# Optimization experiments

Hardware: AMD Instinct MI355X
Metric: run time of the kernel (lower is better)

The kernel has to match this reference:

```python
import jax, jax.numpy as jnp
import numpy as np

N_NODES = 50000
N_EDGES = 819200  # divisible by num_rels=8 -> equal relation segments (implicit rel_ptr)
NUM_RELS = 8
N_HEADS = 4
IN_FEAT = 256
OUT_FEAT = 128
HEAD_DIM = OUT_FEAT // N_HEADS
LEAKY_SLOPE = 0.2


def setup_inputs() -> dict:
    key = jax.random.key(0)
    ks = jax.random.split(key, 7)
    inputs = jax.random.normal(ks[0], (N_NODES, IN_FEAT), dtype=jnp.float32)
    conv_weights = jax.random.normal(ks[1], (NUM_RELS, N_HEADS, IN_FEAT, HEAD_DIM), dtype=jnp.float32) * (1.0 / np.sqrt(IN_FEAT))
    attn_l = jax.random.normal(ks[2], (NUM_RELS, N_HEADS, HEAD_DIM), dtype=jnp.float32) * 0.1
    attn_r = jax.random.normal(ks[3], (NUM_RELS, N_HEADS, HEAD_DIM), dtype=jnp.float32) * 0.1
    h_bias = jax.random.normal(ks[4], (OUT_FEAT,), dtype=jnp.float32) * 0.01
    row_idx = jax.random.randint(ks[5], (N_EDGES,), 0, N_NODES, dtype=jnp.int32)
    col_idx = jax.random.randint(ks[6], (N_EDGES,), 0, N_NODES, dtype=jnp.int32)
    return {
        'inputs': inputs,
        'conv_weights': conv_weights,
        'attn_l': attn_l,
        'attn_r': attn_r,
        'h_bias': h_bias,
        'row_idx': row_idx,
        'col_idx': col_idx,
    }


def reference(inputs, conv_weights, attn_l, attn_r, h_bias, row_idx, col_idx):
    R, H, IN, D = conv_weights.shape
    E = row_idx.shape[0]
    N = inputs.shape[0]
    epr = E // R  # edges per relation (equal segments == rel_ptr)

    # relation-grouped GEMM: per-edge transformed src features [R, epr, H, D]
    src = inputs[row_idx].reshape(R, epr, IN)
    feat_src = jnp.einsum('rei,rhid->rehd', src, conv_weights)
    el = jnp.einsum('rehd,rhd->reh', feat_src, attn_l)

    dst = inputs[col_idx].reshape(R, epr, IN)
    feat_dst = jnp.einsum('rei,rhid->rehd', dst, conv_weights)
    er = jnp.einsum('rehd,rhd->reh', feat_dst, attn_r)

    # fused GAT: leaky_relu(el+er), softmax over incoming edges per dst node
    e = jax.nn.leaky_relu((el + er).reshape(E, H), negative_slope=LEAKY_SLOPE)
    m = jax.ops.segment_max(e, col_idx, num_segments=N)          # [N, H]
    e_exp = jnp.exp(e - m[col_idx])                              # [E, H]
    denom = jax.ops.segment_sum(e_exp, col_idx, num_segments=N)  # [N, H]
    alpha = e_exp / denom[col_idx]                               # [E, H]

    feat = feat_src.reshape(E, H, D)
    h = jax.ops.segment_sum(alpha[:, :, None] * feat, col_idx, num_segments=N)  # [N, H, D]
    h = h.reshape(N, H * D) + h_bias
    # activation=None, self_loop=False, dropout treated as eval (identity)
    return h
```

## Files before the change

### kernel.cpp

```cpp
#include <hip/hip_runtime.h>
#include <hip/hip_bf16.h>

#define N_NODES 50000
#define N_EDGES 819200
#define NUM_RELS 8
#define EPR (N_EDGES / NUM_RELS)
#define N_HEADS 4
#define IN_FEAT 256
#define OUT_FEAT 128
#define HEAD_DIM 32
#define NB_SCAN ((N_NODES + 255) / 256)

typedef __attribute__((ext_vector_type(8))) __bf16 bf16x8;
typedef __attribute__((ext_vector_type(4))) __bf16 bf16x4;
typedef __attribute__((ext_vector_type(4))) float f32x4;

#define SZ_FEAT ((size_t)NUM_RELS * N_NODES * OUT_FEAT)
#define SZ_EL ((size_t)NUM_RELS * N_NODES * N_HEADS)
#define SZ_WB ((size_t)IN_FEAT * 64)
#define SZ_WT ((size_t)NUM_RELS * OUT_FEAT * IN_FEAT / 2)
#define OFF_FEAT ((size_t)0)
#define OFF_EL (OFF_FEAT + SZ_FEAT)
#define OFF_ER (OFF_EL + SZ_EL)
#define OFF_WB (OFF_ER + SZ_EL)
#define OFF_WT (OFF_WB + SZ_WB)
#define OFF_INT (OFF_WT + SZ_WT)
#define IOFF_CNT ((size_t)0)
#define IOFF_PTR ((size_t)N_NODES)
#define IOFF_CUR ((size_t)2 * N_NODES)
#define IOFF_BSUM ((size_t)3 * N_NODES)
#define IOFF_SPAY ((size_t)3 * N_NODES + 256)

__global__ void k_wboth(const float* __restrict__ cw, const float* __restrict__ al,
                        const float* __restrict__ ar, __bf16* __restrict__ wbt) {
    int tid = blockIdx.x * blockDim.x + threadIdx.x;
    if (tid >= IN_FEAT * 64) return;
    int col = tid >> 8, i = tid & 255;
    int side = col >> 5, r = (col >> 2) & 7, h = col & 3;
    const float* av = (side ? ar : al) + (size_t)(r * N_HEADS + h) * HEAD_DIM;
    const float* cwp = cw + ((size_t)(r * N_HEADS + h) * IN_FEAT + i) * HEAD_DIM;
    float s = 0.f;
#pragma unroll
    for (int d = 0; d < HEAD_DIM; ++d) s += cwp[d] * av[d];
    wbt[(size_t)col * IN_FEAT + i] = (__bf16)s;
}

__global__ void k_cvt_w(const float* __restrict__ cw, __bf16* __restrict__ wt) {
    int tid = blockIdx.x * blockDim.x + threadIdx.x;
    if (tid >= NUM_RELS * N_HEADS * IN_FEAT * HEAD_DIM) return;
    int d = tid & 31, k = (tid >> 5) & 255, h = (tid >> 13) & 3, r = tid >> 15;
    float v = cw[tid];
    wt[((size_t)(r * OUT_FEAT + h * HEAD_DIM + d)) * IN_FEAT + k] = (__bf16)v;
}

__global__ __launch_bounds__(256) void k_tmfma(const float* __restrict__ x,
                                               const __bf16* __restrict__ wt,
                                               __bf16* __restrict__ featb) {
    __shared__ __align__(16) unsigned char sA[16384];
    __shared__ __align__(16) unsigned char sB[16384];
    const int t = threadIdx.x;
    const int lane = t & 63, w = t >> 6;
    const int n0 = blockIdx.x * 128;
    const int r = blockIdx.y;
    const int wr = w >> 1, wc = w & 1;

    f32x4 acc[4][4];
#pragma unroll
    for (int i = 0; i < 4; ++i)
#pragma unroll
        for (int j = 0; j < 4; ++j) acc[i][j] = (f32x4){0.f, 0.f, 0.f, 0.f};

    const __bf16* wtr = wt + (size_t)r * OUT_FEAT * IN_FEAT;

    for (int kc = 0; kc < 4; ++kc) {
#pragma unroll
        for (int i = 0; i < 8; ++i) {
            int flat = i * 64 + lane;
            int row = w * 32 + (flat >> 4);
            int kq = flat & 15;
            int nsrc = n0 + row;
            if (nsrc >= N_NODES) nsrc = N_NODES - 1;
            float4 v = *(const float4*)(x + (size_t)nsrc * IN_FEAT + kc * 64 + kq * 4);
            bf16x4 hv;
            hv[0] = (__bf16)v.x; hv[1] = (__bf16)v.y; hv[2] = (__bf16)v.z; hv[3] = (__bf16)v.w;
            int slot = (kq >> 1) ^ (row & 7);
            *(bf16x4*)(sA + row * 128 + slot * 16 + (kq & 1) * 8) = hv;
        }
#pragma unroll
        for (int i = 0; i < 4; ++i) {
            int flat = i * 64 + lane;
            int row = w * 32 + (flat >> 3);
            int s = flat & 7;
            int ssrc = s ^ (row & 7);
            bf16x8 v = *(const bf16x8*)(wtr + (size_t)row * IN_FEAT + kc * 64 + ssrc * 8);
            *(bf16x8*)(sB + row * 128 + s * 16) = v;
        }
        __syncthreads();
#pragma unroll
        for (int ks = 0; ks < 2; ++ks) {
            bf16x8 af[4], bg[4];
#pragma unroll
            for (int rb = 0; rb < 4; ++rb) {
                int row = wr * 64 + rb * 16 + (lane & 15);
                int slot = (ks * 4 + (lane >> 4)) ^ (row & 7);
                af[rb] = *(const bf16x8*)(sA + row * 128 + slot * 16);
            }
#pragma unroll
            for (int cb = 0; cb < 4; ++cb) {
                int row = wc * 64 + cb * 16 + (lane & 15);
                int slot = (ks * 4 + (lane >> 4)) ^ (row & 7);
                bg[cb] = *(const bf16x8*)(sB + row * 128 + slot * 16);
            }
#pragma unroll
            for (int rb = 0; rb < 4; ++rb)
#pragma unroll
                for (int cb = 0; cb < 4; ++cb)
                    acc[rb][cb] = __builtin_amdgcn_mfma_f32_16x16x32_bf16(af[rb], bg[cb], acc[rb][cb], 0, 0, 0);
        }
        __syncthreads();
    }
#pragma unroll
    for (int rb = 0; rb < 4; ++rb) {
#pragma unroll
        for (int q = 0; q < 4; ++q) {
            int row = wr * 64 + rb * 16 + (lane >> 4) * 4 + q;
            int n = n0 + row;
            if (n < N_NODES) {
                __bf16* fp = featb + ((size_t)r * N_NODES + n) * OUT_FEAT + wc * 64 + (lane & 15);
#pragma unroll
                for (int cb = 0; cb < 4; ++cb) fp[cb * 16] = (__bf16)acc[rb][cb][q];
            }
        }
    }
}

__global__ __launch_bounds__(256) void k_elrm(const float* __restrict__ x,
                                              const __bf16* __restrict__ wbt,
                                              float* __restrict__ el,
                                              float* __restrict__ er) {
    __shared__ __align__(16) unsigned char sA[16384];
    __shared__ __align__(16) unsigned char sB[32768];
    const int t = threadIdx.x;
    const int lane = t & 63, w = t >> 6;
    const int n0 = blockIdx.x * 128;

#pragma unroll
    for (int i = 0; i < 8; ++i) {
        int flat = i * 256 + t;
        int row = flat >> 5;
        int s = flat & 31;
        int ssrc = (s & ~7) | ((s & 7) ^ (row & 7));
        bf16x8 v = *(const bf16x8*)(wbt + (size_t)row * IN_FEAT + ssrc * 8);
        *(bf16x8*)(sB + row * 512 + s * 16) = v;
    }

    f32x4 acc[2][4];
#pragma unroll
    for (int i = 0; i < 2; ++i)
#pragma unroll
        for (int j = 0; j < 4; ++j) acc[i][j] = (f32x4){0.f, 0.f, 0.f, 0.f};

    for (int kc = 0; kc < 4; ++kc) {
#pragma unroll
        for (int i = 0; i < 8; ++i) {
            int flat = i * 256 + t;
            int row = flat >> 4;
            int kq = flat & 15;
            int n = n0 + row;
            if (n >= N_NODES) n = N_NODES - 1;
            float4 v = *(const float4*)(x + (size_t)n * IN_FEAT + kc * 64 + kq * 4);
            bf16x4 hv;
            hv[0] = (__bf16)v.x; hv[1] = (__bf16)v.y; hv[2] = (__bf16)v.z; hv[3] = (__bf16)v.w;
            int slot = (kq >> 1) ^ (row & 7);
            *(bf16x4*)(sA + row * 128 + slot * 16 + (kq & 1) * 8) = hv;
        }
        __syncthreads();
#pragma unroll
        for (int ks = 0; ks < 2; ++ks) {
            bf16x8 af[2], bg[4];
#pragma unroll
            for (int rb = 0; rb < 2; ++rb) {
                int row = w * 32 + rb * 16 + (lane & 15);
                int slot = (ks * 4 + (lane >> 4)) ^ (row & 7);
                af[rb] = *(const bf16x8*)(sA + row * 128 + slot * 16);
            }
#pragma unroll
            for (int cb = 0; cb < 4; ++cb) {
                int row = cb * 16 + (lane & 15);
                int slot = kc * 8 + ((ks * 4 + (lane >> 4)) ^ (row & 7));
                bg[cb] = *(const bf16x8*)(sB + row * 512 + slot * 16);
            }
#pragma unroll
            for (int rb = 0; rb < 2; ++rb)
#pragma unroll
                for (int cb = 0; cb < 4; ++cb)
                    acc[rb][cb] = __builtin_amdgcn_mfma_f32_16x16x32_bf16(af[rb], bg[cb], acc[rb][cb], 0, 0, 0);
        }
        __syncthreads();
    }
#pragma unroll
    for (int rb = 0; rb < 2; ++rb) {
#pragma unroll
        for (int q = 0; q < 4; ++q) {
            int n = n0 + w * 32 + rb * 16 + (lane >> 4) * 4 + q;
            if (n < N_NODES) {
#pragma unroll
                for (int cb = 0; cb < 4; ++cb) {
                    int c = cb * 16 + (lane & 15);
                    int side = c >> 5, rr = (c >> 2) & 7, h = c & 3;
                    float* dst = side ? er : el;
                    dst[((size_t)rr * N_NODES + n) * N_HEADS + h] = acc[rb][cb][q];
                }
            }
        }
    }
}

__global__ void k_hist(const int* __restrict__ col, int* __restrict__ cnt) {
    int e = blockIdx.x * blockDim.x + threadIdx.x;
    if (e < N_EDGES) atomicAdd(cnt + col[e], 1);
}

__global__ __launch_bounds__(256) void k_scanA(const int* __restrict__ cnt,
                                               int* __restrict__ excl,
                                               int* __restrict__ bsum) {
    __shared__ int s[256];
    int i = blockIdx.x * 256 + threadIdx.x;
    int v = (i < N_NODES) ? cnt[i] : 0;
    s[threadIdx.x] = v;
    __syncthreads();
#pragma unroll
    for (int off = 1; off < 256; off <<= 1) {
        int t = (threadIdx.x >= off) ? s[threadIdx.x - off] : 0;
        __syncthreads();
        s[threadIdx.x] += t;
        __syncthreads();
    }
    if (i < N_NODES) excl[i] = s[threadIdx.x] - v;
    if (threadIdx.x == 255) bsum[blockIdx.x] = s[255];
}

__global__ __launch_bounds__(256) void k_scanB(int* __restrict__ bsum) {
    __shared__ int s[256];
    int v = (threadIdx.x < NB_SCAN) ? bsum[threadIdx.x] : 0;
    s[threadIdx.x] = v;
    __syncthreads();
#pragma unroll
    for (int off = 1; off < 256; off <<= 1) {
        int t = (threadIdx.x >= off) ? s[threadIdx.x - off] : 0;
        __syncthreads();
        s[threadIdx.x] += t;
        __syncthreads();
    }
    bsum[threadIdx.x] = s[threadIdx.x] - v;
}

__global__ __launch_bounds__(256) void k_scanC(int* __restrict__ ptr,
                                               int* __restrict__ cursor,
                                               const int* __restrict__ bsum) {
    int i = blockIdx.x * 256 + threadIdx.x;
    if (i >= N_NODES) return;
    int p = ptr[i] + bsum[blockIdx.x];
    ptr[i] = p;
    cursor[i] = p;
}

__global__ void k_scatter(const int* __restrict__ row, const int* __restrict__ col,
                          int* __restrict__ cursor, int* __restrict__ spay) {
    int e = blockIdx.x * blockDim.x + threadIdx.x;
    if (e >= N_EDGES) return;
    int c = col[e];
    int pos = atomicAdd(cursor + c, 1);
    spay[pos] = row[e] | ((e / EPR) << 20);
}

__global__ __launch_bounds__(256) void k_agg(const int* __restrict__ ptr,
                                             const int* __restrict__ cnt,
                                             const int* __restrict__ spay,
                                             const float* __restrict__ el,
                                             const float* __restrict__ er,
                                             const __bf16* __restrict__ featb,
                                             const float* __restrict__ bias,
                                             float* __restrict__ out) {
    const int wv = threadIdx.x >> 6, lane = threadIdx.x & 63;
    const int n = blockIdx.x * 4 + wv;
    if (n >= N_NODES) return;
    const int start = ptr[n], len = cnt[n];
    const int h = lane >> 4;
    float accx = 0.f, accy = 0.f, den = 0.f;
    int j = 0;
    for (; j + 4 <= len; j += 4) {
        int p[4];
#pragma unroll
        for (int u = 0; u < 4; ++u) p[u] = spay[start + j + u];
        float w[4], vx[4], vy[4];
#pragma unroll
        for (int u = 0; u < 4; ++u) {
            int rw = p[u] & 0xFFFFF, r = p[u] >> 20;
            size_t rb = (size_t)r * N_NODES;
            float s = el[(rb + rw) * N_HEADS + h] + er[(rb + n) * N_HEADS + h];
            s = s > 0.f ? s : 0.2f * s;
            w[u] = __expf(s);
            ushort2 raw = *(const ushort2*)(featb + (rb + rw) * OUT_FEAT + lane * 2);
            vx[u] = __uint_as_float((unsigned)raw.x << 16);
            vy[u] = __uint_as_float((unsigned)raw.y << 16);
        }
#pragma unroll
        for (int u = 0; u < 4; ++u) {
            accx += w[u] * vx[u];
            accy += w[u] * vy[u];
            den += w[u];
        }
    }
    for (; j < len; ++j) {
        int p = spay[start + j];
        int rw = p & 0xFFFFF, r = p >> 20;
        size_t rb = (size_t)r * N_NODES;
        float s = el[(rb + rw) * N_HEADS + h] + er[(rb + n) * N_HEADS + h];
        s = s > 0.f ? s : 0.2f * s;
        float w = __expf(s);
        ushort2 raw = *(const ushort2*)(featb + (rb + rw) * OUT_FEAT + lane * 2);
        accx += w * __uint_as_float((unsigned)raw.x << 16);
        accy += w * __uint_as_float((unsigned)raw.y << 16);
        den += w;
    }
    float inv = (len > 0) ? 1.f / den : 0.f;
    int o = lane * 2;
    float2 res;
    res.x = accx * inv + bias[o];
    res.y = accy * inv + bias[o + 1];
    *(float2*)(out + (size_t)n * OUT_FEAT + o) = res;
}

extern "C" void kernel_launch(void* const* d_in, const int* in_sizes, int n_in,
                              void* d_out, int out_size, void* d_ws, size_t ws_size,
                              hipStream_t stream) {
    const float* x = (const float*)d_in[0];
    const float* cw = (const float*)d_in[1];
    const float* al = (const float*)d_in[2];
    const float* ar = (const float*)d_in[3];
    const float* bias = (const float*)d_in[4];
    const int* row = (const int*)d_in[5];
    const int* col = (const int*)d_in[6];
    float* out = (float*)d_out;
    float* ws = (float*)d_ws;

    __bf16* featb = (__bf16*)(ws + OFF_FEAT);
    float* el = ws + OFF_EL;
    float* er = ws + OFF_ER;
    __bf16* wbt = (__bf16*)(ws + OFF_WB);
    __bf16* wt = (__bf16*)(ws + OFF_WT);
    int* iw = (int*)(ws + OFF_INT);
    int* cnt = iw + IOFF_CNT;
    int* ptr = iw + IOFF_PTR;
    int* cur = iw + IOFF_CUR;
    int* bsum = iw + IOFF_BSUM;
    int* spay = iw + IOFF_SPAY;

    hipMemsetAsync(cnt, 0, N_NODES * sizeof(int), stream);

    k_wboth<<<(IN_FEAT * 64 + 255) / 256, 256, 0, stream>>>(cw, al, ar, wbt);
    k_cvt_w<<<(NUM_RELS * N_HEADS * IN_FEAT * HEAD_DIM + 255) / 256, 256, 0, stream>>>(cw, wt);
    k_tmfma<<<dim3((N_NODES + 127) / 128, NUM_RELS), 256, 0, stream>>>(x, wt, featb);
    k_elrm<<<(N_NODES + 127) / 128, 256, 0, stream>>>(x, wbt, el, er);

    k_hist<<<(N_EDGES + 255) / 256, 256, 0, stream>>>(col, cnt);
    k_scanA<<<NB_SCAN, 256, 0, stream>>>(cnt, ptr, bsum);
    k_scanB<<<1, 256, 0, stream>>>(bsum);
    k_scanC<<<NB_SCAN, 256, 0, stream>>>(ptr, cur, bsum);
    k_scatter<<<(N_EDGES + 255) / 256, 256, 0, stream>>>(row, col, cur, spay);

    k_agg<<<(N_NODES + 3) / 4, 256, 0, stream>>>(ptr, cnt, spay, el, er, featb, bias, out);
}
```

Measured before the change: 256.0 us.

## Fuse per-relation feature GEMM and attention-logit GEMM into one node-tiled kernel

Merges the per-relation feature GEMM and the el/er logit GEMM into a single kernel. Each block loads and converts its 128-row input tile to bf16 once into 64KB of shared memory, then loops over all 8 relations and finally the logit weights. This removes the repeated global reads and conversions of x, which were done once per relation plus once more for the logits. In exchange the grid shrinks from 391x8 blocks to 391, and the larger shared-memory footprint lowers occupancy, so there is less parallelism for hiding latency.

```diff
diff --git a/kernel.cpp b/kernel.cpp
--- a/kernel.cpp
+++ b/kernel.cpp
@@ -53,68 +53,129 @@
     wt[((size_t)(r * OUT_FEAT + h * HEAD_DIM + d)) * IN_FEAT + k] = (__bf16)v;
 }
 
-__global__ __launch_bounds__(256) void k_tmfma(const float* __restrict__ x,
+__global__ __launch_bounds__(256) void k_fused(const float* __restrict__ x,
                                                const __bf16* __restrict__ wt,
-                                               __bf16* __restrict__ featb) {
-    __shared__ __align__(16) unsigned char sA[16384];
+                                               const __bf16* __restrict__ wbt,
+                                               __bf16* __restrict__ featb,
+                                               float* __restrict__ el,
+                                               float* __restrict__ er) {
+    __shared__ __align__(16) unsigned char sA[65536];
     __shared__ __align__(16) unsigned char sB[16384];
     const int t = threadIdx.x;
-    const int lane = t & 63, w = t >> 6;
+    const int lane = t & 63;
+    const int w = t >> 6;
+    const int wr = w >> 1, wc = w & 1;
     const int n0 = blockIdx.x * 128;
-    const int r = blockIdx.y;
-    const int wr = w >> 1, wc = w & 1;
+
+#pragma unroll 8
+    for (int i = 0; i < 32; ++i) {
+        int flat = i * 256 + t;
+        int row = flat >> 6;
+        int kq = flat & 63;
+        int n = n0 + row;
+        if (n >= N_NODES) n = N_NODES - 1;
+        float4 v = *(const float4*)(x + (size_t)n * IN_FEAT + kq * 4);
+        bf16x4 hv;
+        hv[0] = (__bf16)v.x; hv[1] = (__bf16)v.y; hv[2] = (__bf16)v.z; hv[3] = (__bf16)v.w;
+        int sg = kq >> 1;
+        int slot = (sg & ~7) | ((sg & 7) ^ (row & 7));
+        *(bf16x4*)(sA + row * 512 + slot * 16 + (kq & 1) * 8) = hv;
+    }
+    __syncthreads();
 
     f32x4 acc[4][4];
+
+    for (int r = 0; r < NUM_RELS; ++r) {
+#pragma unroll
+        for (int i = 0; i < 4; ++i)
+#pragma unroll
+            for (int j = 0; j < 4; ++j) acc[i][j] = (f32x4){0.f, 0.f, 0.f, 0.f};
+        const __bf16* wtr = wt + (size_t)r * OUT_FEAT * IN_FEAT;
+
+        for (int kc = 0; kc < 4; ++kc) {
+#pragma unroll
+            for (int i = 0; i < 4; ++i) {
+                int flat = i * 256 + t;
+                int brow = flat >> 3;
+                int s = flat & 7;
+                int ssrc = s ^ (brow & 7);
+                bf16x8 v = *(const bf16x8*)(wtr + (size_t)brow * IN_FEAT + kc * 64 + ssrc * 8);
+                *(bf16x8*)(sB + brow * 128 + s * 16) = v;
+            }
+            __syncthreads();
+#pragma unroll
+            for (int ks = 0; ks < 2; ++ks) {
+                bf16x8 af[4], bg[4];
+#pragma unroll
+                for (int rb = 0; rb < 4; ++rb) {
+                    int row = wr * 64 + rb * 16 + (lane & 15);
+                    int slot = kc * 8 + ((ks * 4 + (lane >> 4)) ^ (row & 7));
+                    af[rb] = *(const bf16x8*)(sA + row * 512 + slot * 16);
+                }
+#pragma unroll
+                for (int cb = 0; cb < 4; ++cb) {
+                    int brow = wc * 64 + cb * 16 + (lane & 15);
+                    int slot = (ks * 4 + (lane >> 4)) ^ (brow & 7);
+                    bg[cb] = *(const bf16x8*)(sB + brow * 128 + slot * 16);
+                }
+#pragma unroll
+                for (int rb = 0; rb < 4; ++rb)
+#pragma unroll
+                    for (int cb = 0; cb < 4; ++cb)
+                        acc[rb][cb] = __builtin_amdgcn_mfma_f32_16x16x32_bf16(af[rb], bg[cb], acc[rb][cb], 0, 0, 0);
+            }
+            __syncthreads();
+        }
+#pragma unroll
+        for (int rb = 0; rb < 4; ++rb) {
+#pragma unroll
+            for (int q = 0; q < 4; ++q) {
+                int row = wr * 64 + rb * 16 + (lane >> 4) * 4 + q;
+                int n = n0 + row;
+                if (n < N_NODES) {
+                    __bf16* fp = featb + ((size_t)r * N_NODES + n) * OUT_FEAT + wc * 64 + (lane & 15);
+#pragma unroll
+                    for (int cb = 0; cb < 4; ++cb) fp[cb * 16] = (__bf16)acc[rb][cb][q];
+                }
+            }
+        }
+    }
+
 #pragma unroll
     for (int i = 0; i < 4; ++i)
 #pragma unroll
-        for (int j = 0; j < 4; ++j) acc[i][j] = (f32x4){0.f, 0.f, 0.f, 0.f};
-
-    const __bf16* wtr = wt + (size_t)r * OUT_FEAT * IN_FEAT;
+        for (int j = 0; j < 2; ++j) acc[i][j] = (f32x4){0.f, 0.f, 0.f, 0.f};
 
     for (int kc = 0; kc < 4; ++kc) {
 #pragma unroll
-        for (int i = 0; i < 8; ++i) {
-            int flat = i * 64 + lane;
-            int row = w * 32 + (flat >> 4);
-            int kq = flat & 15;
-            int nsrc = n0 + row;
-            if (nsrc >= N_NODES) nsrc = N_NODES - 1;
-            float4 v = *(const float4*)(x + (size_t)nsrc * IN_FEAT + kc * 64 + kq * 4);
-            bf16x4 hv;
-            hv[0] = (__bf16)v.x; hv[1] = (__bf16)v.y; hv[2] = (__bf16)v.z; hv[3] = (__bf16)v.w;
-            int slot = (kq >> 1) ^ (row & 7);
-            *(bf16x4*)(sA + row * 128 + slot * 16 + (kq & 1) * 8) = hv;
-        }
-#pragma unroll
-        for (int i = 0; i < 4; ++i) {
-            int flat = i * 64 + lane;
-            int row = w * 32 + (flat >> 3);
+        for (int i = 0; i < 2; ++i) {
+            int flat = i * 256 + t;
+            int brow = flat >> 3;
             int s = flat & 7;
-            int ssrc = s ^ (row & 7);
-            bf16x8 v = *(const bf16x8*)(wtr + (size_t)row * IN_FEAT + kc * 64 + ssrc * 8);
-            *(bf16x8*)(sB + row * 128 + s * 16) = v;
+            int ssrc = s ^ (brow & 7);
+            bf16x8 v = *(const bf16x8*)(wbt + (size_t)brow * IN_FEAT + kc * 64 + ssrc * 8);
+            *(bf16x8*)(sB + brow * 128 + s * 16) = v;
         }
         __syncthreads();
 #pragma unroll
         for (int ks = 0; ks < 2; ++ks) {
-            bf16x8 af[4], bg[4];
+            bf16x8 af[4], bg[2];
 #pragma unroll
             for (int rb = 0; rb < 4; ++rb) {
                 int row = wr * 64 + rb * 16 + (lane & 15);
-                int slot = (ks * 4 + (lane >> 4)) ^ (row & 7);
-                af[rb] = *(const bf16x8*)(sA + row * 128 + slot * 16);
-            }
-#pragma unroll
-            for (int cb = 0; cb < 4; ++cb) {
-                int row = wc * 64 + cb * 16 + (lane & 15);
-                int slot = (ks * 4 + (lane >> 4)) ^ (row & 7);
-                bg[cb] = *(const bf16x8*)(sB + row * 128 + slot * 16);
+                int slot = kc * 8 + ((ks * 4 + (lane >> 4)) ^ (row & 7));
+                af[rb] = *(const bf16x8*)(sA + row * 512 + slot * 16);
+            }
+#pragma unroll
+            for (int cb = 0; cb < 2; ++cb) {
+                int brow = wc * 32 + cb * 16 + (lane & 15);
+                int slot = (ks * 4 + (lane >> 4)) ^ (brow & 7);
+                bg[cb] = *(const bf16x8*)(sB + brow * 128 + slot * 16);
             }
 #pragma unroll
             for (int rb = 0; rb < 4; ++rb)
 #pragma unroll
-                for (int cb = 0; cb < 4; ++cb)
+                for (int cb = 0; cb < 2; ++cb)
                     acc[rb][cb] = __builtin_amdgcn_mfma_f32_16x16x32_bf16(af[rb], bg[cb], acc[rb][cb], 0, 0, 0);
         }
         __syncthreads();
@@ -123,90 +184,11 @@
     for (int rb = 0; rb < 4; ++rb) {
 #pragma unroll
         for (int q = 0; q < 4; ++q) {
-            int row = wr * 64 + rb * 16 + (lane >> 4) * 4 + q;
-            int n = n0 + row;
+            int n = n0 + wr * 64 + rb * 16 + (lane >> 4) * 4 + q;
             if (n < N_NODES) {
-                __bf16* fp = featb + ((size_t)r * N_NODES + n) * OUT_FEAT + wc * 64 + (lane & 15);
-#pragma unroll
-                for (int cb = 0; cb < 4; ++cb) fp[cb * 16] = (__bf16)acc[rb][cb][q];
-            }
-        }
-    }
-}
-
-__global__ __launch_bounds__(256) void k_elrm(const float* __restrict__ x,
-                                              const __bf16* __restrict__ wbt,
-                                              float* __restrict__ el,
-                                              float* __restrict__ er) {
-    __shared__ __align__(16) unsigned char sA[16384];
-    __shared__ __align__(16) unsigned char sB[32768];
-    const int t = threadIdx.x;
-    const int lane = t & 63, w = t >> 6;
-    const int n0 = blockIdx.x * 128;
-
-#pragma unroll
-    for (int i = 0; i < 8; ++i) {
-        int flat = i * 256 + t;
-        int row = flat >> 5;
-        int s = flat & 31;
-        int ssrc = (s & ~7) | ((s & 7) ^ (row & 7));
-        bf16x8 v = *(const bf16x8*)(wbt + (size_t)row * IN_FEAT + ssrc * 8);
-        *(bf16x8*)(sB + row * 512 + s * 16) = v;
-    }
-
-    f32x4 acc[2][4];
-#pragma unroll
-    for (int i = 0; i < 2; ++i)
-#pragma unroll
-        for (int j = 0; j < 4; ++j) acc[i][j] = (f32x4){0.f, 0.f, 0.f, 0.f};
-
-    for (int kc = 0; kc < 4; ++kc) {
-#pragma unroll
-        for (int i = 0; i < 8; ++i) {
-            int flat = i * 256 + t;
-            int row = flat >> 4;
-            int kq = flat & 15;
-            int n = n0 + row;
-            if (n >= N_NODES) n = N_NODES - 1;
-            float4 v = *(const float4*)(x + (size_t)n * IN_FEAT + kc * 64 + kq * 4);
-            bf16x4 hv;
-            hv[0] = (__bf16)v.x; hv[1] = (__bf16)v.y; hv[2] = (__bf16)v.z; hv[3] = (__bf16)v.w;
-            int slot = (kq >> 1) ^ (row & 7);
-            *(bf16x4*)(sA + row * 128 + slot * 16 + (kq & 1) * 8) = hv;
-        }
-        __syncthreads();
-#pragma unroll
-        for (int ks = 0; ks < 2; ++ks) {
-            bf16x8 af[2], bg[4];
-#pragma unroll
-            for (int rb = 0; rb < 2; ++rb) {
-                int row = w * 32 + rb * 16 + (lane & 15);
-                int slot = (ks * 4 + (lane >> 4)) ^ (row & 7);
-                af[rb] = *(const bf16x8*)(sA + row * 128 + slot * 16);
-            }
-#pragma unroll
-            for (int cb = 0; cb < 4; ++cb) {
-                int row = cb * 16 + (lane & 15);
-                int slot = kc * 8 + ((ks * 4 + (lane >> 4)) ^ (row & 7));
-                bg[cb] = *(const bf16x8*)(sB + row * 512 + slot * 16);
-            }
-#pragma unroll
-            for (int rb = 0; rb < 2; ++rb)
-#pragma unroll
-                for (int cb = 0; cb < 4; ++cb)
-                    acc[rb][cb] = __builtin_amdgcn_mfma_f32_16x16x32_bf16(af[rb], bg[cb], acc[rb][cb], 0, 0, 0);
-        }
-        __syncthreads();
-    }
-#pragma unroll
-    for (int rb = 0; rb < 2; ++rb) {
-#pragma unroll
-        for (int q = 0; q < 4; ++q) {
-            int n = n0 + w * 32 + rb * 16 + (lane >> 4) * 4 + q;
-            if (n < N_NODES) {
-#pragma unroll
-                for (int cb = 0; cb < 4; ++cb) {
-                    int c = cb * 16 + (lane & 15);
+#pragma unroll
+                for (int cb = 0; cb < 2; ++cb) {
+                    int c = wc * 32 + cb * 16 + (lane & 15);
                     int side = c >> 5, rr = (c >> 2) & 7, h = c & 3;
                     float* dst = side ? er : el;
                     dst[((size_t)rr * N_NODES + n) * N_HEADS + h] = acc[rb][cb][q];
@@ -361,8 +343,7 @@
 
     k_wboth<<<(IN_FEAT * 64 + 255) / 256, 256, 0, stream>>>(cw, al, ar, wbt);
     k_cvt_w<<<(NUM_RELS * N_HEADS * IN_FEAT * HEAD_DIM + 255) / 256, 256, 0, stream>>>(cw, wt);
-    k_tmfma<<<dim3((N_NODES + 127) / 128, NUM_RELS), 256, 0, stream>>>(x, wt, featb);
-    k_elrm<<<(N_NODES + 127) / 128, 256, 0, stream>>>(x, wbt, el, er);
+    k_fused<<<(N_NODES + 127) / 128, 256, 0, stream>>>(x, wt, wbt, featb, el, er);
 
     k_hist<<<(N_EDGES + 255) / 256, 256, 0, stream>>>(col, cnt);
     k_scanA<<<NB_SCAN, 256, 0, stream>>>(cnt, ptr, bsum);
```

Result: faster. 213.4 us (-16.6%).
